# Kernel optimization log

Measured on AMD Instinct MI355X. Metric: run time of the kernel, lower is better.

Reference implementation:

```python
import jax, jax.numpy as jnp
import numpy as np

N = 100000
E = 1600000
C = 64        # in_channels == out_channels
P = 3         # phys_dim
H = 64        # hidden_mlp_dim
EPS = 1e-5

def _glorot(key, shape):
    fan_in = shape[0]
    return jax.random.normal(key, shape, dtype=jnp.float32) / jnp.sqrt(jnp.float32(fan_in))

def setup_inputs() -> dict:
    key = jax.random.key(0)
    ks = jax.random.split(key, 20)
    inp = {
        'x': jax.random.normal(ks[0], (N, C), dtype=jnp.float32),
        'pos': jax.random.normal(ks[1], (N, P), dtype=jnp.float32),
        'edge_index': jax.random.randint(ks[2], (2, E), 0, N, dtype=jnp.int32),
        # lin_in
        'W_in': _glorot(ks[3], (C, C)), 'b_in': jnp.zeros((C,), jnp.float32),
        # pre_attn_norm (LayerNorm)
        'ln_g': jnp.ones((C,), jnp.float32), 'ln_b': jnp.zeros((C,), jnp.float32),
        # PointTransformerConv linears (no bias, as in PyG)
        'W_lin': _glorot(ks[4], (C, C)),
        'W_src': _glorot(ks[5], (C, C)),
        'W_dst': _glorot(ks[6], (C, C)),
        # pos_nn: MLP [P, H, C], act after both layers (plain_last=False)
        'pn_W1': _glorot(ks[7], (P, H)), 'pn_b1': jnp.zeros((H,), jnp.float32),
        'pn_W2': _glorot(ks[8], (H, C)), 'pn_b2': jnp.zeros((C,), jnp.float32),
        # attn_nn: MLP [C, H, C]
        'an_W1': _glorot(ks[9], (C, H)), 'an_b1': jnp.zeros((H,), jnp.float32),
        'an_W2': _glorot(ks[10], (H, C)), 'an_b2': jnp.zeros((C,), jnp.float32),
        # lin_out
        'W_out': _glorot(ks[11], (C, C)), 'b_out': jnp.zeros((C,), jnp.float32),
    }
    return inp

def _mlp2(h, W1, b1, W2, b2):
    # two Linear layers, ReLU after each (plain_last=False, norm=None)
    return jax.nn.relu(jax.nn.relu(h @ W1 + b1) @ W2 + b2)

def reference(x, pos, edge_index, W_in, b_in, ln_g, ln_b, W_lin, W_src, W_dst,
              pn_W1, pn_b1, pn_W2, pn_b2, an_W1, an_b1, an_W2, an_b2, W_out, b_out):
    n = x.shape[0]
    src = edge_index[0]  # j (source)
    dst = edge_index[1]  # i (target)

    # lin_in + act
    h = jax.nn.relu(x @ W_in + b_in)
    # layernorm
    mu = jnp.mean(h, axis=-1, keepdims=True)
    var = jnp.mean((h - mu) ** 2, axis=-1, keepdims=True)
    h = (h - mu) * jax.lax.rsqrt(var + EPS) * ln_g + ln_b

    # PointTransformerConv
    q = h @ W_dst   # alpha_i source
    k = h @ W_src   # alpha_j source
    v = h @ W_lin   # value

    delta = _mlp2(pos[dst] - pos[src], pn_W1, pn_b1, pn_W2, pn_b2)  # (E, C)
    alpha = _mlp2(q[dst] - k[src] + delta, an_W1, an_b1, an_W2, an_b2)  # (E, C)

    # per-destination, per-channel segment softmax
    m = jax.ops.segment_max(alpha, dst, num_segments=n)        # (N, C), -inf for empty
    e = jnp.exp(alpha - m[dst])
    s = jax.ops.segment_sum(e, dst, num_segments=n)
    w = e / (s[dst] + 1e-16)

    out = jax.ops.segment_sum(w * (v[src] + delta), dst, num_segments=n)  # (N, C)

    # lin_out + act
    return jax.nn.relu(out @ W_out + b_out)
```

## Files before the change

kernel.cpp:

```cpp
#include <hip/hip_runtime.h>


typedef __bf16 bf16x8 __attribute__((ext_vector_type(8)));
typedef float f32x4 __attribute__((ext_vector_type(4)));

#define SRT_SH   7
#define SRT_CAP  2560
#define SRT_EPB  16384

__device__ inline unsigned short f2bf(float f) {
  return __builtin_bit_cast(unsigned short, (__bf16)f);
}
__device__ inline float bf2f(unsigned short s) {
  return __uint_as_float(((unsigned int)s) << 16);
}
__device__ inline bf16x8 ld_bf8(const unsigned short* p) {
  union { uint4 i; bf16x8 v; } u;
  u.i = *(const uint4*)p;
  return u.v;
}
__device__ inline unsigned int cvt_pk_bf16(float lo, float hi) {
  unsigned int r;
  asm("v_cvt_pk_bf16_f32 %0, %1, %2" : "=v"(r) : "v"(lo), "v"(hi));
  return r;
}


__global__ __launch_bounds__(256) void k_prep(
    const float* __restrict__ W_in, const float* __restrict__ W_dst,
    const float* __restrict__ W_src, const float* __restrict__ W_lin,
    const float* __restrict__ pn_W2, const float* __restrict__ an_W1,
    const float* __restrict__ an_W2, const float* __restrict__ W_out,
    unsigned short* __restrict__ wt) {
  int t = threadIdx.x;
  const float* Ws[8] = {W_in, W_dst, W_src, W_lin, pn_W2, an_W1, an_W2, W_out};
  const float* W = Ws[blockIdx.x];
  unsigned short* o = wt + (size_t)blockIdx.x * 4608;
#pragma unroll
  for (int i = 0; i < 16; ++i) {
    int e = i * 256 + t;
    int k = e >> 6, n = e & 63;
    o[n * 72 + k] = f2bf(W[e]);
  }
}


__global__ __launch_bounds__(256) void k_s1(
    const int* __restrict__ src, const int* __restrict__ dst, int E, int CB,
    int* __restrict__ ccnt, int2* __restrict__ pcoarse) {
  __shared__ int hist[1024];
  __shared__ int offs[1024];
  __shared__ int cur[1024];
  int t = threadIdx.x;
  for (int i = t; i < 1024; i += 256) { hist[i] = 0; cur[i] = 0; }
  __syncthreads();
  long e0 = (long)blockIdx.x * SRT_EPB;
  int nE = (int)(((long)E - e0) < SRT_EPB ? ((long)E - e0) : SRT_EPB);
  for (int i = t; i < nE; i += 256)
    atomicAdd(&hist[dst[e0 + i] >> SRT_SH], 1);
  __syncthreads();
  for (int k = t; k < CB; k += 256) {
    int h = hist[k];
    offs[k] = (h > 0) ? atomicAdd(&ccnt[k], h) : 0;
  }
  __syncthreads();
  for (int i = t; i < nE; i += 256) {
    int s = src[e0 + i], d = dst[e0 + i];
    int k = d >> SRT_SH;
    int p = offs[k] + atomicAdd(&cur[k], 1);
    if (p < SRT_CAP) pcoarse[(size_t)k * SRT_CAP + p] = make_int2(s, d);
  }
}

__global__ __launch_bounds__(256) void k_s1scan(
    const int* __restrict__ ccnt, int* __restrict__ cbase, int CB) {
  __shared__ int sd[256];
  int t = threadIdx.x;
  int v[4]; int ts = 0;
#pragma unroll
  for (int i = 0; i < 4; ++i) {
    int idx = t * 4 + i;
    int c = (idx < CB) ? min(ccnt[idx], SRT_CAP) : 0;
    v[i] = c; ts += c;
  }
  sd[t] = ts;
  __syncthreads();
  for (int off = 1; off < 256; off <<= 1) {
    int xv = (t >= off) ? sd[t - off] : 0;
    __syncthreads();
    sd[t] += xv;
    __syncthreads();
  }
  int run = sd[t] - ts;
#pragma unroll
  for (int i = 0; i < 4; ++i) {
    int idx = t * 4 + i;
    if (idx < CB) cbase[idx] = run;
    run += v[i];
  }
}


__global__ __launch_bounds__(256) void k_s2(
    const int2* __restrict__ pcoarse, const int* __restrict__ ccnt,
    const int* __restrict__ cbase, int2* __restrict__ spair) {
  __shared__ int dh[128], dcur[128], dbase[128], sd[128];
  int t = threadIdx.x;
  int k = blockIdx.x;
  if (t < 128) { dh[t] = 0; dcur[t] = 0; }
  __syncthreads();
  int cnt = min(ccnt[k], SRT_CAP);
  const int2* bb = pcoarse + (size_t)k * SRT_CAP;
  int dlo = k << SRT_SH;
  for (int i = t; i < cnt; i += 256)
    atomicAdd(&dh[bb[i].y - dlo], 1);
  __syncthreads();
  if (t < 128) sd[t] = dh[t];
  __syncthreads();
  for (int off = 1; off < 128; off <<= 1) {
    int xv = 0;
    if (t < 128 && t >= off) xv = sd[t - off];
    __syncthreads();
    if (t < 128) sd[t] += xv;
    __syncthreads();
  }
  if (t < 128) dbase[t] = cbase[k] + sd[t] - dh[t];
  __syncthreads();
  for (int i = t; i < cnt; i += 256) {
    int2 e = bb[i];
    int j = e.y - dlo;
    int p = dbase[j] + atomicAdd(&dcur[j], 1);
    spair[p] = e;
  }
}


__global__ __launch_bounds__(256) void k_node(
    const float* __restrict__ x, const unsigned short* __restrict__ wt,
    const float* __restrict__ b_in, const float* __restrict__ ln_g,
    const float* __restrict__ ln_b,
    unsigned short* __restrict__ qg, unsigned short* __restrict__ kg,
    unsigned short* __restrict__ vg, int N) {
  int t = threadIdx.x;

  __shared__ __align__(16) unsigned short WALL[4 * 64 * 72];
  __shared__ __align__(16) unsigned short HT[64 * 72];
  __shared__ __align__(16) float LNG[64], LNB[64], BIN[64];

  int lane = t & 63, wv = t >> 6;
  int nl = lane & 15, q = lane >> 4;
  int w16 = wv * 16;
  int n0g = blockIdx.x * 64;

  {
    const uint4* s4 = (const uint4*)wt;
    uint4* d4 = (uint4*)WALL;
#pragma unroll
    for (int i = 0; i < 9; ++i) d4[i * 256 + t] = s4[i * 256 + t];
  }
  if (t < 64) { LNG[t] = ln_g[t]; LNB[t] = ln_b[t]; BIN[t] = b_in[t]; }

  int row = n0g + w16 + nl;
  bf16x8 b[2];
#pragma unroll
  for (int s = 0; s < 2; ++s) {
    union { unsigned int u[4]; bf16x8 v; } fb;
    if (row < N) {
      int kb = s * 32 + q * 8;
      float4 xa = *(const float4*)(x + (size_t)row * 64 + kb);
      float4 xb = *(const float4*)(x + (size_t)row * 64 + kb + 4);
      fb.u[0] = cvt_pk_bf16(xa.x, xa.y);
      fb.u[1] = cvt_pk_bf16(xa.z, xa.w);
      fb.u[2] = cvt_pk_bf16(xb.x, xb.y);
      fb.u[3] = cvt_pk_bf16(xb.z, xb.w);
    } else {
#pragma unroll
      for (int j = 0; j < 4; ++j) fb.u[j] = 0;
    }
    b[s] = fb.v;
  }
  __syncthreads();

  f32x4 h[4];
#pragma unroll
  for (int m0 = 0; m0 < 4; ++m0) {
    f32x4 acc = *(const f32x4*)&BIN[m0 * 16 + q * 4];
    acc = __builtin_amdgcn_mfma_f32_16x16x32_bf16(
        ld_bf8(&WALL[(m0 * 16 + nl) * 72 + q * 8]), b[0], acc, 0, 0, 0);
    acc = __builtin_amdgcn_mfma_f32_16x16x32_bf16(
        ld_bf8(&WALL[(m0 * 16 + nl) * 72 + 32 + q * 8]), b[1], acc, 0, 0, 0);
#pragma unroll
    for (int r = 0; r < 4; ++r) acc[r] = fmaxf(acc[r], 0.f);
    h[m0] = acc;
  }

  float sv = 0.f, sq = 0.f;
#pragma unroll
  for (int m0 = 0; m0 < 4; ++m0)
#pragma unroll
    for (int r = 0; r < 4; ++r) {
      float v = h[m0][r];
      sv += v; sq += v * v;
    }
  sv += __shfl_xor(sv, 16); sq += __shfl_xor(sq, 16);
  sv += __shfl_xor(sv, 32); sq += __shfl_xor(sq, 32);
  float mu = sv * (1.f / 64.f);
  float var = sq * (1.f / 64.f) - mu * mu;
  float rs = rsqrtf(var + 1e-5f);
#pragma unroll
  for (int m0 = 0; m0 < 4; ++m0) {
    f32x4 g4 = *(const f32x4*)&LNG[m0 * 16 + q * 4];
    f32x4 o4 = *(const f32x4*)&LNB[m0 * 16 + q * 4];
    float v0 = (h[m0][0] - mu) * rs * g4[0] + o4[0];
    float v1 = (h[m0][1] - mu) * rs * g4[1] + o4[1];
    float v2 = (h[m0][2] - mu) * rs * g4[2] + o4[2];
    float v3 = (h[m0][3] - mu) * rs * g4[3] + o4[3];
    uint2 pk;
    pk.x = cvt_pk_bf16(v0, v1);
    pk.y = cvt_pk_bf16(v2, v3);
    *(uint2*)&HT[(w16 + nl) * 72 + m0 * 16 + q * 4] = pk;
  }

  b[0] = ld_bf8(&HT[(w16 + nl) * 72 + q * 8]);
  b[1] = ld_bf8(&HT[(w16 + nl) * 72 + 32 + q * 8]);

  unsigned short* Og[3] = {qg, kg, vg};
  bool g = row < N;
#pragma unroll
  for (int m = 0; m < 3; ++m) {
    const unsigned short* Wm = WALL + (m + 1) * 4608;
#pragma unroll
    for (int m0 = 0; m0 < 4; ++m0) {
      f32x4 acc = {0.f, 0.f, 0.f, 0.f};
      acc = __builtin_amdgcn_mfma_f32_16x16x32_bf16(
          ld_bf8(&Wm[(m0 * 16 + nl) * 72 + q * 8]), b[0], acc, 0, 0, 0);
      acc = __builtin_amdgcn_mfma_f32_16x16x32_bf16(
          ld_bf8(&Wm[(m0 * 16 + nl) * 72 + 32 + q * 8]), b[1], acc, 0, 0, 0);
      if (g) {
        uint2 pk;
        pk.x = cvt_pk_bf16(acc[0], acc[1]);
        pk.y = cvt_pk_bf16(acc[2], acc[3]);
        int off = (m == 2) ? (q * 16 + m0 * 4) : (m0 * 16 + q * 4);
        *(uint2*)(Og[m] + (size_t)row * 64 + off) = pk;
      }
    }
  }
}


__global__ __launch_bounds__(256, 4) void k_edge(
    const int2* __restrict__ spair, const float* __restrict__ pos,
    const unsigned short* __restrict__ qg, const unsigned short* __restrict__ kg,
    const unsigned short* __restrict__ vg,
    const unsigned short* __restrict__ wt,
    const float* __restrict__ pn_W1, const float* __restrict__ pn_b1,
    const float* __restrict__ pn_b2,
    const float* __restrict__ an_b1, const float* __restrict__ an_b2,
    float* __restrict__ sg, float* __restrict__ accg, int E, int numTiles) {
  __shared__ __align__(16) unsigned short WAB[2 * 64 * 72];
  __shared__ __align__(16) unsigned short SD[64 * 72];
  __shared__ __align__(16) unsigned short SB[64 * 72];
  __shared__ float W1[3 * 64];
  __shared__ float B1[64];
  __shared__ __align__(16) float B2[64], AB1[64], AB2[64];

  int t = threadIdx.x;
  int lane = t & 63, wv = t >> 6;
  int nl = lane & 15, q = lane >> 4;
  int w16 = wv * 16;

  {
    const uint4* s4 = (const uint4*)(wt + 4 * 4608);
    uint4* d4 = (uint4*)WAB;
#pragma unroll
    for (int i = 0; i < 5; ++i) {
      int idx = i * 256 + t;
      if (idx < 1152) d4[idx] = s4[idx];
    }
  }
  if (t < 192) W1[t] = pn_W1[t];
  if (t < 64) {
    B1[t] = pn_b1[t];  B2[t] = pn_b2[t];
    AB1[t] = an_b1[t]; AB2[t] = an_b2[t];
  }
  bf16x8 wan2r[8];
#pragma unroll
  for (int m0 = 0; m0 < 4; ++m0)
#pragma unroll
    for (int s = 0; s < 2; ++s)
      wan2r[m0 * 2 + s] =
          ld_bf8(wt + 6 * 4608 + (m0 * 16 + nl) * 72 + s * 32 + q * 8);
  const unsigned short* WPN2 = WAB;
  const unsigned short* WAN1 = WAB + 4608;
  __syncthreads();

  long er_off = w16 + nl;
  int2 my;
  {
    long er = (long)blockIdx.x * 64 + er_off;
    my = (er < E) ? spair[er] : make_int2(0, 0);
  }

  for (int tile = blockIdx.x; tile < numTiles; tile += gridDim.x) {
    long e0 = (long)tile * 64;

    const unsigned short* qr = qg + (size_t)my.y * 64;
    const unsigned short* kr = kg + (size_t)my.x * 64;
    bf16x8 qf[2], kf[2];
#pragma unroll
    for (int s = 0; s < 2; ++s) {
      int kb = s * 32 + q * 8;
      qf[s] = ld_bf8(qr + kb);
      kf[s] = ld_bf8(kr + kb);
    }
    const unsigned short* vr = vg + (size_t)my.x * 64;
    bf16x8 vlo = ld_bf8(vr + q * 16);
    bf16x8 vhi = ld_bf8(vr + q * 16 + 8);
    float p0 = pos[my.y * 3 + 0] - pos[my.x * 3 + 0];
    float p1 = pos[my.y * 3 + 1] - pos[my.x * 3 + 1];
    float p2 = pos[my.y * 3 + 2] - pos[my.x * 3 + 2];

    int2 nxt = make_int2(0, 0);
    {
      long ntile = (long)tile + gridDim.x;
      if (ntile < numTiles) {
        long ner = ntile * 64 + er_off;
        nxt = (ner < E) ? spair[ner] : make_int2(0, 0);
      }
    }

    bool elive = (e0 + er_off) < E;

    bf16x8 b[2];

#pragma unroll
    for (int s = 0; s < 2; ++s) {
      union { unsigned int u[4]; bf16x8 v; } fb;
      int kb = s * 32 + q * 8;
#pragma unroll
      for (int jj = 0; jj < 4; ++jj) {
        int c0 = kb + 2 * jj, c1 = c0 + 1;
        float v0 = fmaf(p0, W1[c0],
                   fmaf(p1, W1[64 + c0],
                   fmaf(p2, W1[128 + c0], B1[c0])));
        float v1 = fmaf(p0, W1[c1],
                   fmaf(p1, W1[64 + c1],
                   fmaf(p2, W1[128 + c1], B1[c1])));
        fb.u[jj] = cvt_pk_bf16(fmaxf(v0, 0.f), fmaxf(v1, 0.f));
      }
      b[s] = fb.v;
    }

    f32x4 dlt[4];
#pragma unroll
    for (int m0 = 0; m0 < 4; ++m0) {
      f32x4 acc = *(const f32x4*)&B2[m0 * 16 + q * 4];
      acc = __builtin_amdgcn_mfma_f32_16x16x32_bf16(
          ld_bf8(&WPN2[(m0 * 16 + nl) * 72 + q * 8]), b[0], acc, 0, 0, 0);
      acc = __builtin_amdgcn_mfma_f32_16x16x32_bf16(
          ld_bf8(&WPN2[(m0 * 16 + nl) * 72 + 32 + q * 8]), b[1], acc, 0, 0, 0);
#pragma unroll
      for (int r = 0; r < 4; ++r) acc[r] = fmaxf(acc[r], 0.f);
      dlt[m0] = acc;
      uint2 pk;
      pk.x = cvt_pk_bf16(acc[0], acc[1]);
      pk.y = cvt_pk_bf16(acc[2], acc[3]);
      *(uint2*)&SD[(w16 + nl) * 72 + m0 * 16 + q * 4] = pk;
    }

#pragma unroll
    for (int s = 0; s < 2; ++s) {
      int kb = s * 32 + q * 8;
      bf16x8 d8 = ld_bf8(&SD[(w16 + nl) * 72 + kb]);
      union { unsigned int u[4]; bf16x8 v; } fb;
#pragma unroll
      for (int jj = 0; jj < 4; ++jj) {
        float v0 = (float)qf[s][2 * jj]     - (float)kf[s][2 * jj]     + (float)d8[2 * jj];
        float v1 = (float)qf[s][2 * jj + 1] - (float)kf[s][2 * jj + 1] + (float)d8[2 * jj + 1];
        fb.u[jj] = cvt_pk_bf16(v0, v1);
      }
      b[s] = fb.v;
    }

#pragma unroll
    for (int m0 = 0; m0 < 4; ++m0) {
      float va0, va1, va2, va3;
      if (m0 == 0)      { va0 = (float)vlo[0]; va1 = (float)vlo[1];
                          va2 = (float)vlo[2]; va3 = (float)vlo[3]; }
      else if (m0 == 1) { va0 = (float)vlo[4]; va1 = (float)vlo[5];
                          va2 = (float)vlo[6]; va3 = (float)vlo[7]; }
      else if (m0 == 2) { va0 = (float)vhi[0]; va1 = (float)vhi[1];
                          va2 = (float)vhi[2]; va3 = (float)vhi[3]; }
      else              { va0 = (float)vhi[4]; va1 = (float)vhi[5];
                          va2 = (float)vhi[6]; va3 = (float)vhi[7]; }
      uint2 pk;
      pk.x = cvt_pk_bf16(dlt[m0][0] + va0, dlt[m0][1] + va1);
      pk.y = cvt_pk_bf16(dlt[m0][2] + va2, dlt[m0][3] + va3);
      *(uint2*)&SD[(w16 + nl) * 72 + m0 * 16 + q * 4] = pk;
    }

#pragma unroll
    for (int m0 = 0; m0 < 4; ++m0) {
      f32x4 acc = *(const f32x4*)&AB1[m0 * 16 + q * 4];
      acc = __builtin_amdgcn_mfma_f32_16x16x32_bf16(
          ld_bf8(&WAN1[(m0 * 16 + nl) * 72 + q * 8]), b[0], acc, 0, 0, 0);
      acc = __builtin_amdgcn_mfma_f32_16x16x32_bf16(
          ld_bf8(&WAN1[(m0 * 16 + nl) * 72 + 32 + q * 8]), b[1], acc, 0, 0, 0);
      uint2 pk;
      pk.x = cvt_pk_bf16(fmaxf(acc[0], 0.f), fmaxf(acc[1], 0.f));
      pk.y = cvt_pk_bf16(fmaxf(acc[2], 0.f), fmaxf(acc[3], 0.f));
      *(uint2*)&SB[(w16 + nl) * 72 + m0 * 16 + q * 4] = pk;
    }

    b[0] = ld_bf8(&SB[(w16 + nl) * 72 + q * 8]);
    b[1] = ld_bf8(&SB[(w16 + nl) * 72 + 32 + q * 8]);
#pragma unroll
    for (int m0 = 0; m0 < 4; ++m0) {
      f32x4 acc = *(const f32x4*)&AB2[m0 * 16 + q * 4];
      acc = __builtin_amdgcn_mfma_f32_16x16x32_bf16(
          wan2r[m0 * 2 + 0], b[0], acc, 0, 0, 0);
      acc = __builtin_amdgcn_mfma_f32_16x16x32_bf16(
          wan2r[m0 * 2 + 1], b[1], acc, 0, 0, 0);
      float e0v = elive ? __expf(fmaxf(acc[0], 0.f)) : 0.f;
      float e1v = elive ? __expf(fmaxf(acc[1], 0.f)) : 0.f;
      float e2v = elive ? __expf(fmaxf(acc[2], 0.f)) : 0.f;
      float e3v = elive ? __expf(fmaxf(acc[3], 0.f)) : 0.f;
      uint2 pk;
      pk.x = cvt_pk_bf16(e0v, e1v);
      pk.y = cvt_pk_bf16(e2v, e3v);
      *(uint2*)&SB[(w16 + nl) * 72 + m0 * 16 + q * 4] = pk;
    }

    {
      int c = lane;
      int cur = __shfl(my.y, 0);
      float ssum = 0.f, asum = 0.f;
#pragma unroll
      for (int i = 0; i < 16; ++i) {
        int d = __shfl(my.y, i);
        if (d != cur) {
          if (ssum != 0.f) {
            atomicAdd(&sg[(size_t)cur * 64 + c], ssum);
            atomicAdd(&accg[(size_t)cur * 64 + c], asum);
          }
          cur = d; ssum = 0.f; asum = 0.f;
        }
        float ex = bf2f(SB[(w16 + i) * 72 + c]);
        float pay = bf2f(SD[(w16 + i) * 72 + c]);
        ssum += ex;
        asum = fmaf(ex, pay, asum);
      }
      if (ssum != 0.f) {
        atomicAdd(&sg[(size_t)cur * 64 + c], ssum);
        atomicAdd(&accg[(size_t)cur * 64 + c], asum);
      }
    }

    my = nxt;
  }
}


__global__ __launch_bounds__(256) void k_out(const float* __restrict__ accg,
                                             const float* __restrict__ sg,
                                             const unsigned short* __restrict__ wt,
                                             const float* __restrict__ b,
                                             float* __restrict__ out, int N) {
  __shared__ __align__(16) unsigned short WO[64 * 72];
  __shared__ __align__(16) float BO[64];
  int t = threadIdx.x;
  int lane = t & 63, wv = t >> 6;
  int nl = lane & 15, q = lane >> 4;
  int w16 = wv * 16;
  int n0g = blockIdx.x * 64;

  {
    const uint4* s4 = (const uint4*)(wt + 7 * 4608);
    uint4* d4 = (uint4*)WO;
#pragma unroll
    for (int i = 0; i < 3; ++i) {
      int idx = i * 256 + t;
      if (idx < 576) d4[idx] = s4[idx];
    }
  }
  if (t < 64) BO[t] = b[t];

  int row = n0g + w16 + nl;
  bf16x8 bb[2];
#pragma unroll
  for (int s = 0; s < 2; ++s) {
    union { unsigned int u[4]; bf16x8 v; } fb;
    if (row < N) {
      int kb = s * 32 + q * 8;
      float4 na = *(const float4*)(accg + (size_t)row * 64 + kb);
      float4 nb = *(const float4*)(accg + (size_t)row * 64 + kb + 4);
      float4 da = *(const float4*)(sg + (size_t)row * 64 + kb);
      float4 db = *(const float4*)(sg + (size_t)row * 64 + kb + 4);
      fb.u[0] = cvt_pk_bf16(na.x / (da.x + 1e-16f), na.y / (da.y + 1e-16f));
      fb.u[1] = cvt_pk_bf16(na.z / (da.z + 1e-16f), na.w / (da.w + 1e-16f));
      fb.u[2] = cvt_pk_bf16(nb.x / (db.x + 1e-16f), nb.y / (db.y + 1e-16f));
      fb.u[3] = cvt_pk_bf16(nb.z / (db.z + 1e-16f), nb.w / (db.w + 1e-16f));
    } else {
#pragma unroll
      for (int j = 0; j < 4; ++j) fb.u[j] = 0;
    }
    bb[s] = fb.v;
  }
  __syncthreads();

  bool g = row < N;
#pragma unroll
  for (int m0 = 0; m0 < 4; ++m0) {
    f32x4 acc = *(const f32x4*)&BO[m0 * 16 + q * 4];
    acc = __builtin_amdgcn_mfma_f32_16x16x32_bf16(
        ld_bf8(&WO[(m0 * 16 + nl) * 72 + q * 8]), bb[0], acc, 0, 0, 0);
    acc = __builtin_amdgcn_mfma_f32_16x16x32_bf16(
        ld_bf8(&WO[(m0 * 16 + nl) * 72 + 32 + q * 8]), bb[1], acc, 0, 0, 0);
    if (g) {
      float4 o;
      o.x = fmaxf(acc[0], 0.f);
      o.y = fmaxf(acc[1], 0.f);
      o.z = fmaxf(acc[2], 0.f);
      o.w = fmaxf(acc[3], 0.f);
      *(float4*)(out + (size_t)row * 64 + m0 * 16 + q * 4) = o;
    }
  }
}


extern "C" void kernel_launch(void* const* d_in, const int* in_sizes, int n_in,
                              void* d_out, int out_size, void* d_ws, size_t ws_size,
                              hipStream_t stream) {
  const float* x     = (const float*)d_in[0];
  const float* pos   = (const float*)d_in[1];
  const int*   eidx  = (const int*)d_in[2];
  const float* W_in  = (const float*)d_in[3];
  const float* b_in  = (const float*)d_in[4];
  const float* ln_g  = (const float*)d_in[5];
  const float* ln_b  = (const float*)d_in[6];
  const float* W_lin = (const float*)d_in[7];
  const float* W_src = (const float*)d_in[8];
  const float* W_dst = (const float*)d_in[9];
  const float* pn_W1 = (const float*)d_in[10];
  const float* pn_b1 = (const float*)d_in[11];
  const float* pn_W2 = (const float*)d_in[12];
  const float* pn_b2 = (const float*)d_in[13];
  const float* an_W1 = (const float*)d_in[14];
  const float* an_b1 = (const float*)d_in[15];
  const float* an_W2 = (const float*)d_in[16];
  const float* an_b2 = (const float*)d_in[17];
  const float* W_out = (const float*)d_in[18];
  const float* b_out = (const float*)d_in[19];
  float* out = (float*)d_out;

  int N = in_sizes[0] / 64;
  int E = in_sizes[2] / 2;
  const int* src = eidx;
  const int* dst = eidx + E;

  char* w = (char*)d_ws;
  auto alloc = [&](size_t bytes) -> void* {
    void* p = (void*)w;
    w += (bytes + 255) & ~(size_t)255;
    return p;
  };
  unsigned short* qg = (unsigned short*)alloc((size_t)N * 64 * 2);
  unsigned short* kg = (unsigned short*)alloc((size_t)N * 64 * 2);
  unsigned short* vg = (unsigned short*)alloc((size_t)N * 64 * 2);
  float* sg   = (float*)alloc((size_t)N * 64 * 4);
  float* accg = (float*)alloc((size_t)N * 64 * 4);
  int2* spair = (int2*)alloc((size_t)E * 8);
  unsigned short* wt = (unsigned short*)alloc(8 * 4608 * 2);
  int* ccnt  = (int*)alloc(1024 * 4);
  int* cbase = (int*)alloc(1024 * 4);
  int2* pcoarse = (int2*)sg;

  int CB = (N + 127) >> SRT_SH;
  int s1Blocks = (E + SRT_EPB - 1) / SRT_EPB;
  int nodeBlocks = (N + 63) / 64;
  int numTiles = (E + 63) / 64;
  int edgeGrid = numTiles < 1024 ? numTiles : 1024;

  hipMemsetAsync(ccnt, 0, 1024 * 4, stream);
  k_prep<<<8, 256, 0, stream>>>(
      W_in, W_dst, W_src, W_lin, pn_W2, an_W1, an_W2, W_out, wt);
  k_s1<<<s1Blocks, 256, 0, stream>>>(src, dst, E, CB, ccnt, pcoarse);
  k_s1scan<<<1, 256, 0, stream>>>(ccnt, cbase, CB);
  k_s2<<<CB, 256, 0, stream>>>(pcoarse, ccnt, cbase, spair);
  hipMemsetAsync(sg, 0, (size_t)N * 64 * 4 * 2, stream);
  k_node<<<nodeBlocks, 256, 0, stream>>>(
      x, wt, b_in, ln_g, ln_b, qg, kg, vg, N);
  k_edge<<<edgeGrid, 256, 0, stream>>>(spair, pos, qg, kg, vg, wt,
                                       pn_W1, pn_b1, pn_b2, an_b1, an_b2,
                                       sg, accg, E, numTiles);
  k_out<<<nodeBlocks, 256, 0, stream>>>(accg, sg, wt, b_out, out, N);
}
```

Before: 386.9 us.

## Merge sort, node and zeroing stages into fewer kernel launches

Removes both hipMemsetAsync calls: the ccnt clear moves into an extra k_prep block, and the sg/accg clear moves into extra blocks of the second-pass sort kernel. The coarse edge-bucketing pass and the node projection kernel now share one launch, with blocks split by block index and a common shared-memory buffer. Because sg is now zeroed while pcoarse is still being read, pcoarse gets its own workspace allocation instead of aliasing sg. The aim is fewer launches and gaps between launches, and letting independent work overlap. The cost is extra workspace memory, and the bucketing blocks now reserve the node kernel's larger shared-memory footprint.

```diff
diff --git a/kernel.cpp b/kernel.cpp
--- a/kernel.cpp
+++ b/kernel.cpp
@@ -31,8 +31,13 @@
     const float* __restrict__ W_src, const float* __restrict__ W_lin,
     const float* __restrict__ pn_W2, const float* __restrict__ an_W1,
     const float* __restrict__ an_W2, const float* __restrict__ W_out,
-    unsigned short* __restrict__ wt) {
+    unsigned short* __restrict__ wt, int* __restrict__ ccnt) {
   int t = threadIdx.x;
+  if (blockIdx.x == 8) {
+    if (t < 256) { ccnt[t] = 0; ccnt[256 + t] = 0; ccnt[512 + t] = 0;
+                   ccnt[768 + t] = 0; }
+    return;
+  }
   const float* Ws[8] = {W_in, W_dst, W_src, W_lin, pn_W2, an_W1, an_W2, W_out};
   const float* W = Ws[blockIdx.x];
   unsigned short* o = wt + (size_t)blockIdx.x * 4608;
@@ -45,112 +50,52 @@
 }
 
 
-__global__ __launch_bounds__(256) void k_s1(
+__global__ __launch_bounds__(256) void k_s1_node(
     const int* __restrict__ src, const int* __restrict__ dst, int E, int CB,
-    int* __restrict__ ccnt, int2* __restrict__ pcoarse) {
-  __shared__ int hist[1024];
-  __shared__ int offs[1024];
-  __shared__ int cur[1024];
-  int t = threadIdx.x;
-  for (int i = t; i < 1024; i += 256) { hist[i] = 0; cur[i] = 0; }
-  __syncthreads();
-  long e0 = (long)blockIdx.x * SRT_EPB;
-  int nE = (int)(((long)E - e0) < SRT_EPB ? ((long)E - e0) : SRT_EPB);
-  for (int i = t; i < nE; i += 256)
-    atomicAdd(&hist[dst[e0 + i] >> SRT_SH], 1);
-  __syncthreads();
-  for (int k = t; k < CB; k += 256) {
-    int h = hist[k];
-    offs[k] = (h > 0) ? atomicAdd(&ccnt[k], h) : 0;
-  }
-  __syncthreads();
-  for (int i = t; i < nE; i += 256) {
-    int s = src[e0 + i], d = dst[e0 + i];
-    int k = d >> SRT_SH;
-    int p = offs[k] + atomicAdd(&cur[k], 1);
-    if (p < SRT_CAP) pcoarse[(size_t)k * SRT_CAP + p] = make_int2(s, d);
-  }
-}
-
-__global__ __launch_bounds__(256) void k_s1scan(
-    const int* __restrict__ ccnt, int* __restrict__ cbase, int CB) {
-  __shared__ int sd[256];
-  int t = threadIdx.x;
-  int v[4]; int ts = 0;
-#pragma unroll
-  for (int i = 0; i < 4; ++i) {
-    int idx = t * 4 + i;
-    int c = (idx < CB) ? min(ccnt[idx], SRT_CAP) : 0;
-    v[i] = c; ts += c;
-  }
-  sd[t] = ts;
-  __syncthreads();
-  for (int off = 1; off < 256; off <<= 1) {
-    int xv = (t >= off) ? sd[t - off] : 0;
-    __syncthreads();
-    sd[t] += xv;
-    __syncthreads();
-  }
-  int run = sd[t] - ts;
-#pragma unroll
-  for (int i = 0; i < 4; ++i) {
-    int idx = t * 4 + i;
-    if (idx < CB) cbase[idx] = run;
-    run += v[i];
-  }
-}
-
-
-__global__ __launch_bounds__(256) void k_s2(
-    const int2* __restrict__ pcoarse, const int* __restrict__ ccnt,
-    const int* __restrict__ cbase, int2* __restrict__ spair) {
-  __shared__ int dh[128], dcur[128], dbase[128], sd[128];
-  int t = threadIdx.x;
-  int k = blockIdx.x;
-  if (t < 128) { dh[t] = 0; dcur[t] = 0; }
-  __syncthreads();
-  int cnt = min(ccnt[k], SRT_CAP);
-  const int2* bb = pcoarse + (size_t)k * SRT_CAP;
-  int dlo = k << SRT_SH;
-  for (int i = t; i < cnt; i += 256)
-    atomicAdd(&dh[bb[i].y - dlo], 1);
-  __syncthreads();
-  if (t < 128) sd[t] = dh[t];
-  __syncthreads();
-  for (int off = 1; off < 128; off <<= 1) {
-    int xv = 0;
-    if (t < 128 && t >= off) xv = sd[t - off];
-    __syncthreads();
-    if (t < 128) sd[t] += xv;
-    __syncthreads();
-  }
-  if (t < 128) dbase[t] = cbase[k] + sd[t] - dh[t];
-  __syncthreads();
-  for (int i = t; i < cnt; i += 256) {
-    int2 e = bb[i];
-    int j = e.y - dlo;
-    int p = dbase[j] + atomicAdd(&dcur[j], 1);
-    spair[p] = e;
-  }
-}
-
-
-__global__ __launch_bounds__(256) void k_node(
+    int* __restrict__ ccnt, int2* __restrict__ pcoarse, int s1Blocks,
     const float* __restrict__ x, const unsigned short* __restrict__ wt,
     const float* __restrict__ b_in, const float* __restrict__ ln_g,
     const float* __restrict__ ln_b,
     unsigned short* __restrict__ qg, unsigned short* __restrict__ kg,
     unsigned short* __restrict__ vg, int N) {
+  __shared__ __align__(16) unsigned char SH[46848];
   int t = threadIdx.x;
 
-  __shared__ __align__(16) unsigned short WALL[4 * 64 * 72];
-  __shared__ __align__(16) unsigned short HT[64 * 72];
-  __shared__ __align__(16) float LNG[64], LNB[64], BIN[64];
+  if ((int)blockIdx.x < s1Blocks) {
+    int* hist = (int*)SH;
+    int* offs = hist + 1024;
+    int* cur  = offs + 1024;
+    for (int i = t; i < 1024; i += 256) { hist[i] = 0; cur[i] = 0; }
+    __syncthreads();
+    long e0 = (long)blockIdx.x * SRT_EPB;
+    int nE = (int)(((long)E - e0) < SRT_EPB ? ((long)E - e0) : SRT_EPB);
+    for (int i = t; i < nE; i += 256)
+      atomicAdd(&hist[dst[e0 + i] >> SRT_SH], 1);
+    __syncthreads();
+    for (int k = t; k < CB; k += 256) {
+      int h = hist[k];
+      offs[k] = (h > 0) ? atomicAdd(&ccnt[k], h) : 0;
+    }
+    __syncthreads();
+    for (int i = t; i < nE; i += 256) {
+      int s = src[e0 + i], d = dst[e0 + i];
+      int k = d >> SRT_SH;
+      int p = offs[k] + atomicAdd(&cur[k], 1);
+      if (p < SRT_CAP) pcoarse[(size_t)k * SRT_CAP + p] = make_int2(s, d);
+    }
+    return;
+  }
+
+  unsigned short* WALL = (unsigned short*)SH;
+  unsigned short* HT   = (unsigned short*)(SH + 36864);
+  float* LNG = (float*)(SH + 46080);
+  float* LNB = (float*)(SH + 46336);
+  float* BIN = (float*)(SH + 46592);
 
   int lane = t & 63, wv = t >> 6;
   int nl = lane & 15, q = lane >> 4;
   int w16 = wv * 16;
-  int n0g = blockIdx.x * 64;
+  int n0g = ((int)blockIdx.x - s1Blocks) * 64;
 
   {
     const uint4* s4 = (const uint4*)wt;
@@ -244,6 +189,74 @@
         *(uint2*)(Og[m] + (size_t)row * 64 + off) = pk;
       }
     }
+  }
+}
+
+__global__ __launch_bounds__(256) void k_s1scan(
+    const int* __restrict__ ccnt, int* __restrict__ cbase, int CB) {
+  __shared__ int sd[256];
+  int t = threadIdx.x;
+  int v[4]; int ts = 0;
+#pragma unroll
+  for (int i = 0; i < 4; ++i) {
+    int idx = t * 4 + i;
+    int c = (idx < CB) ? min(ccnt[idx], SRT_CAP) : 0;
+    v[i] = c; ts += c;
+  }
+  sd[t] = ts;
+  __syncthreads();
+  for (int off = 1; off < 256; off <<= 1) {
+    int xv = (t >= off) ? sd[t - off] : 0;
+    __syncthreads();
+    sd[t] += xv;
+    __syncthreads();
+  }
+  int run = sd[t] - ts;
+#pragma unroll
+  for (int i = 0; i < 4; ++i) {
+    int idx = t * 4 + i;
+    if (idx < CB) cbase[idx] = run;
+    run += v[i];
+  }
+}
+
+
+__global__ __launch_bounds__(256) void k_s2_zero(
+    const int2* __restrict__ pcoarse, const int* __restrict__ ccnt,
+    const int* __restrict__ cbase, int2* __restrict__ spair, int CB,
+    float4* __restrict__ zbase, int zcount) {
+  int t = threadIdx.x;
+  if ((int)blockIdx.x >= CB) {
+    int i = ((int)blockIdx.x - CB) * 256 + t;
+    if (i < zcount) zbase[i] = make_float4(0.f, 0.f, 0.f, 0.f);
+    return;
+  }
+  __shared__ int dh[128], dcur[128], dbase[128], sd[128];
+  int k = blockIdx.x;
+  if (t < 128) { dh[t] = 0; dcur[t] = 0; }
+  __syncthreads();
+  int cnt = min(ccnt[k], SRT_CAP);
+  const int2* bb = pcoarse + (size_t)k * SRT_CAP;
+  int dlo = k << SRT_SH;
+  for (int i = t; i < cnt; i += 256)
+    atomicAdd(&dh[bb[i].y - dlo], 1);
+  __syncthreads();
+  if (t < 128) sd[t] = dh[t];
+  __syncthreads();
+  for (int off = 1; off < 128; off <<= 1) {
+    int xv = 0;
+    if (t < 128 && t >= off) xv = sd[t - off];
+    __syncthreads();
+    if (t < 128) sd[t] += xv;
+    __syncthreads();
+  }
+  if (t < 128) dbase[t] = cbase[k] + sd[t] - dh[t];
+  __syncthreads();
+  for (int i = t; i < cnt; i += 256) {
+    int2 e = bb[i];
+    int j = e.y - dlo;
+    int p = dbase[j] + atomicAdd(&dcur[j], 1);
+    spair[p] = e;
   }
 }
 
@@ -573,23 +586,24 @@
   unsigned short* wt = (unsigned short*)alloc(8 * 4608 * 2);
   int* ccnt  = (int*)alloc(1024 * 4);
   int* cbase = (int*)alloc(1024 * 4);
-  int2* pcoarse = (int2*)sg;
+  int2* pcoarse = (int2*)alloc((size_t)1024 * SRT_CAP * 8);
 
   int CB = (N + 127) >> SRT_SH;
   int s1Blocks = (E + SRT_EPB - 1) / SRT_EPB;
   int nodeBlocks = (N + 63) / 64;
+  int zcount = N * 32;
+  int zBlocks = (zcount + 255) / 256;
   int numTiles = (E + 63) / 64;
   int edgeGrid = numTiles < 1024 ? numTiles : 1024;
 
-  hipMemsetAsync(ccnt, 0, 1024 * 4, stream);
-  k_prep<<<8, 256, 0, stream>>>(
-      W_in, W_dst, W_src, W_lin, pn_W2, an_W1, an_W2, W_out, wt);
-  k_s1<<<s1Blocks, 256, 0, stream>>>(src, dst, E, CB, ccnt, pcoarse);
+  k_prep<<<9, 256, 0, stream>>>(
+      W_in, W_dst, W_src, W_lin, pn_W2, an_W1, an_W2, W_out, wt, ccnt);
+  k_s1_node<<<s1Blocks + nodeBlocks, 256, 0, stream>>>(
+      src, dst, E, CB, ccnt, pcoarse, s1Blocks,
+      x, wt, b_in, ln_g, ln_b, qg, kg, vg, N);
   k_s1scan<<<1, 256, 0, stream>>>(ccnt, cbase, CB);
-  k_s2<<<CB, 256, 0, stream>>>(pcoarse, ccnt, cbase, spair);
-  hipMemsetAsync(sg, 0, (size_t)N * 64 * 4 * 2, stream);
-  k_node<<<nodeBlocks, 256, 0, stream>>>(
-      x, wt, b_in, ln_g, ln_b, qg, kg, vg, N);
+  k_s2_zero<<<CB + zBlocks, 256, 0, stream>>>(
+      pcoarse, ccnt, cbase, spair, CB, (float4*)sg, zcount);
   k_edge<<<edgeGrid, 256, 0, stream>>>(spair, pos, qg, kg, vg, wt,
                                        pn_W1, pn_b1, pn_b2, an_b1, an_b2,
                                        sg, accg, E, numTiles);
```

After: 371.3 us. 4.0% less time.
